# Kernel tuning notes

Hardware: AMD Instinct MI355X
Metric: run time of the kernel (lower is better)

Reference implementation:

```python
import jax, jax.numpy as jnp
import numpy as np

B, T, D, HS = 8, 2048, 1024, 64  # batch, seq, num_embd, head_size


def setup_inputs() -> dict:
    key = jax.random.key(0)
    kc, kq, kk, kv = jax.random.split(key, 4)
    return {
        "context": jax.random.normal(kc, (B, T, D), dtype=jnp.float32),
        "Wq": jax.random.normal(kq, (D, HS), dtype=jnp.float32) * (D ** -0.5),
        "Wk": jax.random.normal(kk, (D, HS), dtype=jnp.float32) * (D ** -0.5),
        "Wv": jax.random.normal(kv, (D, HS), dtype=jnp.float32) * (D ** -0.5),
    }


def reference(context, Wq, Wk, Wv):
    # context: [B, T, D]; projections: [B, T, HS]
    q = context @ Wq
    k = context @ Wk
    v = context @ Wv
    scale = k.shape[-1] ** -0.5
    # scores: [B, T, T], causal mask, stable softmax (dropout p=0 -> identity)
    wei = jnp.einsum("btd,bsd->bts", q, k) * scale
    t = wei.shape[-1]
    causal = jnp.tril(jnp.ones((t, t), dtype=bool))
    wei = jnp.where(causal, wei, -jnp.inf)
    wei = jax.nn.softmax(wei, axis=-1)
    return jnp.einsum("bts,bsh->bth", wei, v)
```

## Files before the change

### kernel.cpp

```cpp
#include <hip/hip_runtime.h>
#include <math.h>

#define BB 8
#define TT 2048
#define DD 1024
#define HSZ 64

typedef __bf16 bf16_t;
typedef bf16_t bf16x8 __attribute__((ext_vector_type(8)));
typedef bf16_t bf16x4 __attribute__((ext_vector_type(4)));
typedef float f32x4 __attribute__((ext_vector_type(4)));

#define MFMA16(A, B, C) __builtin_amdgcn_mfma_f32_16x16x32_bf16(A, B, C, 0, 0, 0)


__global__ __launch_bounds__(256) void wt_convert(
    const float* __restrict__ Wq, const float* __restrict__ Wk,
    const float* __restrict__ Wv, bf16_t* __restrict__ Wtf)
{
    int id = blockIdx.x * 256 + threadIdx.x;
    int j = id & 7;
    int lane = (id >> 3) & 63;
    int chunk = (id >> 9) & 31;
    int nt = id >> 14;
    int l16 = lane & 15, quad = lane >> 4;
    int k = chunk * 32 + quad * 8 + j;
    int col = nt * 16 + l16;
    int m = col >> 6, ncol = col & 63;
    const float* W = (m == 0) ? Wq : (m == 1) ? Wk : Wv;
    float scl = (m == 0) ? 0.18033688f : 1.0f;
    Wtf[id] = (bf16_t)(W[k * HSZ + ncol] * scl);
}

__global__ __launch_bounds__(256, 3) void qkv_proj(
    const float* __restrict__ ctx, const bf16_t* __restrict__ Wtf,
    bf16_t* __restrict__ Q, bf16_t* __restrict__ Kf, bf16_t* __restrict__ Vf)
{
    __shared__ f32x4 red[4][12][64];

    const int tid = threadIdx.x;
    const int w = tid >> 6, lane = tid & 63;
    const int quad = lane >> 4, l16 = lane & 15;
    const size_t row0 = (size_t)blockIdx.x * 16;
    const int k0 = w * 256;

    f32x4 acc[12];
    #pragma unroll
    for (int i = 0; i < 12; ++i) acc[i] = (f32x4){0.f, 0.f, 0.f, 0.f};

    const float* arow = ctx + (row0 + l16) * DD + k0 + quad * 8;

    float4 a0 = *(const float4*)(arow);
    float4 a1 = *(const float4*)(arow + 4);
    #pragma unroll
    for (int kc = 0; kc < 256; kc += 32) {
        bf16x8 af;
        af[0] = (bf16_t)a0.x; af[1] = (bf16_t)a0.y;
        af[2] = (bf16_t)a0.z; af[3] = (bf16_t)a0.w;
        af[4] = (bf16_t)a1.x; af[5] = (bf16_t)a1.y;
        af[6] = (bf16_t)a1.z; af[7] = (bf16_t)a1.w;
        if (kc + 32 < 256) {
            a0 = *(const float4*)(arow + kc + 32);
            a1 = *(const float4*)(arow + kc + 36);
        }
        const int chunk = (k0 + kc) >> 5;
        #pragma unroll
        for (int nt = 0; nt < 12; ++nt) {
            const bf16_t* wp = Wtf + (((size_t)nt * 32 + chunk) * 64 + lane) * 8;
            bf16x8 bfrag = *(const bf16x8*)wp;
            acc[nt] = MFMA16(af, bfrag, acc[nt]);
        }
    }

    #pragma unroll
    for (int nt = 0; nt < 12; ++nt) red[w][nt][lane] = acc[nt];
    __syncthreads();

    const int bb   = (int)(row0 >> 11);
    const int tloc = (int)(row0 & 2047);
    const int kt   = tloc >> 6;
    const int nn   = (tloc >> 4) & 3;

    #pragma unroll
    for (int i = 0; i < 3; ++i) {
        const int nt = w * 3 + i;
        f32x4 s = red[0][nt][lane];
        s += red[1][nt][lane];
        s += red[2][nt][lane];
        s += red[3][nt][lane];

        const int m = nt >> 2;
        if (m == 0) {
            const int col = (nt & 3) * 16 + l16;
            #pragma unroll
            for (int reg = 0; reg < 4; ++reg)
                Q[(row0 + quad * 4 + reg) * HSZ + col] = (bf16_t)s[reg];
        } else if (m == 1) {
            const int g = nt - 4;
            const int ks = g >> 1;
            const int quadf = (g & 1) * 2 + (l16 >> 3);
            const int jj = l16 & 7;
            const size_t fb = ((((size_t)bb * 32 + kt) * 4 + nn) * 2 + ks) * 512;
            #pragma unroll
            for (int reg = 0; reg < 4; ++reg)
                Kf[fb + (quadf * 16 + quad * 4 + reg) * 8 + jj] = (bf16_t)s[reg];
        } else {
            const int dt = nt - 8;
            const int t0 = tloc + quad * 4;
            const int ks = (t0 >> 5) & 1;
            const int quadf = (t0 >> 3) & 3;
            const int j0 = t0 & 7;
            const size_t fb = ((((size_t)bb * 32 + kt) * 2 + ks) * 4 + dt) * 512;
            bf16x4 v;
            #pragma unroll
            for (int reg = 0; reg < 4; ++reg) v[reg] = (bf16_t)s[reg];
            *(bf16x4*)(Vf + fb + (quadf * 16 + l16) * 8 + j0) = v;
        }
    }
}

__global__ __launch_bounds__(64, 3) void attn_kernel(
    const bf16_t* __restrict__ Q, const bf16_t* __restrict__ Kf,
    const bf16_t* __restrict__ Vf,
    float* __restrict__ Opart, float* __restrict__ Lpart)
{
    __shared__ bf16_t Ps[16][76];

    const int lane = threadIdx.x;
    const int quad = lane >> 4, l16 = lane & 15;

    const int z = blockIdx.x;
    const int b = z & 7, c = z >> 3;
    const int j = 127 - (c >> 2);
    const int seg = c & 3;
    const size_t base = (size_t)b * TT * HSZ;
    const int ntile = (j >> 2) + 1, jm = j & 3;

    const bf16_t* qp = Q + base + (size_t)(j * 16 + l16) * HSZ + quad * 8;
    bf16x8 qf0 = *(const bf16x8*)qp;
    bf16x8 qf1 = *(const bf16x8*)(qp + 32);

    bf16x8 onesf;
    {
        bf16_t e = (l16 == 0) ? (bf16_t)1.0f : (bf16_t)0.0f;
        #pragma unroll
        for (int i = 0; i < 8; ++i) onesf[i] = e;
    }

    f32x4 o[4];
    #pragma unroll
    for (int dt = 0; dt < 4; ++dt) o[dt] = (f32x4){0.f, 0.f, 0.f, 0.f};
    f32x4 lacc = (f32x4){0.f, 0.f, 0.f, 0.f};

    for (int kt = seg; kt < ntile; kt += 4) {
        const bool last = (kt == ntile - 1);
        const int nv = last ? jm + 1 : 4;
        const int ksm = (nv > 2) ? 2 : 1;

        const bf16_t* kbase = Kf + (((size_t)b * 32 + kt) * 8) * 512 + lane * 8;
        bf16x8 kf[8];
        #pragma unroll
        for (int n = 0; n < 4; ++n) {
            if (n < nv) {
                kf[2 * n]     = *(const bf16x8*)(kbase + (n * 2) * 512);
                kf[2 * n + 1] = *(const bf16x8*)(kbase + (n * 2 + 1) * 512);
            }
        }
        const bf16_t* vbase = Vf + (((size_t)b * 32 + kt) * 8) * 512 + lane * 8;
        bf16x8 vf[8];
        #pragma unroll
        for (int dt = 0; dt < 4; ++dt) {
            vf[2 * dt] = *(const bf16x8*)(vbase + dt * 512);
            if (ksm == 2) vf[2 * dt + 1] = *(const bf16x8*)(vbase + (4 + dt) * 512);
        }

        f32x4 sc[4];
        #pragma unroll
        for (int n = 0; n < 4; ++n) {
            if (n < nv) {
                f32x4 a = (f32x4){0.f, 0.f, 0.f, 0.f};
                a = MFMA16(qf0, kf[2 * n], a);
                a = MFMA16(qf1, kf[2 * n + 1], a);
                sc[n] = a;
            }
        }

        if (last) {
            #pragma unroll
            for (int n = 0; n < 4; ++n) {
                if (n < nv) {
                    #pragma unroll
                    for (int reg = 0; reg < 4; ++reg) {
                        bool masked = (n == jm) && (l16 > quad * 4 + reg);
                        float p = __builtin_amdgcn_exp2f(sc[n][reg]);
                        sc[n][reg] = masked ? 0.f : p;
                    }
                }
            }
        } else {
            #pragma unroll
            for (int n = 0; n < 4; ++n) {
                #pragma unroll
                for (int reg = 0; reg < 4; ++reg)
                    sc[n][reg] = __builtin_amdgcn_exp2f(sc[n][reg]);
            }
        }

        #pragma unroll
        for (int n = 0; n < 4; ++n) {
            #pragma unroll
            for (int reg = 0; reg < 4; ++reg) {
                float p = (n < nv) ? sc[n][reg] : 0.f;
                Ps[quad * 4 + reg][n * 16 + l16] = (bf16_t)p;
            }
        }
        bf16x8 pf0 = *(const bf16x8*)&Ps[l16][quad * 8];
        bf16x8 pf1 = *(const bf16x8*)&Ps[l16][32 + quad * 8];

        #pragma unroll
        for (int dt = 0; dt < 4; ++dt) {
            o[dt] = MFMA16(pf0, vf[2 * dt], o[dt]);
            if (ksm == 2) o[dt] = MFMA16(pf1, vf[2 * dt + 1], o[dt]);
        }
        lacc = MFMA16(pf0, onesf, lacc);
        if (ksm == 2) lacc = MFMA16(pf1, onesf, lacc);
    }

    float* op = Opart + (size_t)z * 16 * 64;
    #pragma unroll
    for (int dt = 0; dt < 4; ++dt) {
        #pragma unroll
        for (int reg = 0; reg < 4; ++reg)
            op[(quad * 4 + reg) * 64 + dt * 16 + l16] = o[dt][reg];
    }
    if (l16 == 0) {
        #pragma unroll
        for (int reg = 0; reg < 4; ++reg)
            Lpart[z * 16 + quad * 4 + reg] = lacc[reg];
    }
}

__global__ __launch_bounds__(256) void combine_kernel(
    const float* __restrict__ Opart, const float* __restrict__ Lpart,
    float* __restrict__ O)
{
    int gid = blockIdx.x * 256 + threadIdx.x;
    int col = gid & 63;
    int row = (gid >> 6) & 15;
    int j   = (gid >> 10) & 127;
    int b   = gid >> 17;
    int z0 = ((127 - j) * 4) * 8 + b;
    float l = 0.f, ov = 0.f;
    #pragma unroll
    for (int s = 0; s < 4; ++s) {
        l  += Lpart[(z0 + 8 * s) * 16 + row];
        ov += Opart[((size_t)(z0 + 8 * s) * 16 + row) * 64 + col];
    }
    O[((size_t)b * TT + j * 16 + row) * 64 + col] = ov / l;
}

extern "C" void kernel_launch(void* const* d_in, const int* in_sizes, int n_in,
                              void* d_out, int out_size, void* d_ws, size_t ws_size,
                              hipStream_t stream) {
    const float* ctx = (const float*)d_in[0];
    const float* Wq  = (const float*)d_in[1];
    const float* Wk  = (const float*)d_in[2];
    const float* Wv  = (const float*)d_in[3];
    float* out = (float*)d_out;

    const size_t NQ = (size_t)BB * TT * HSZ;
    bf16_t* Qw  = (bf16_t*)d_ws;
    bf16_t* Kfw = Qw + NQ;
    bf16_t* Vfw = Kfw + NQ;
    bf16_t* Wtf = Vfw + NQ;
    float*  Opart = (float*)(Wtf + 196608);
    float*  Lpart = Opart + (size_t)4096 * 1024;

    wt_convert<<<768, 256, 0, stream>>>(Wq, Wk, Wv, Wtf);
    qkv_proj<<<1024, 256, 0, stream>>>(ctx, Wtf, Qw, Kfw, Vfw);
    attn_kernel<<<4096, 64, 0, stream>>>(Qw, Kfw, Vfw, Opart, Lpart);
    combine_kernel<<<4096, 256, 0, stream>>>(Opart, Lpart, out);
}
```

Before: 141.6 us.

## Double-buffer weight fragments in QKV projection and K fragments in attention

The QKV projection now prefetches the next chunk's weight fragments into a second register buffer while the MFMAs for the current chunk run, and its occupancy hint drops from 3 to 2 to make room for the extra registers. The attention kernel splits its loop into two K-fragment buffers, loading the next tile's K fragments before processing the current one so global load latency overlaps with compute. The cost is higher register pressure and lower occupancy, which may reduce the latency hiding that came from having more waves resident.

```diff
diff --git a/kernel.cpp b/kernel.cpp
--- a/kernel.cpp
+++ b/kernel.cpp
@@ -32,7 +32,7 @@
     Wtf[id] = (bf16_t)(W[k * HSZ + ncol] * scl);
 }
 
-__global__ __launch_bounds__(256, 3) void qkv_proj(
+__global__ __launch_bounds__(256, 2) void qkv_proj(
     const float* __restrict__ ctx, const bf16_t* __restrict__ Wtf,
     bf16_t* __restrict__ Q, bf16_t* __restrict__ Kf, bf16_t* __restrict__ Vf)
 {
@@ -49,27 +49,40 @@
     for (int i = 0; i < 12; ++i) acc[i] = (f32x4){0.f, 0.f, 0.f, 0.f};
 
     const float* arow = ctx + (row0 + l16) * DD + k0 + quad * 8;
-
+    const bf16_t* wbase = Wtf + lane * 8;
+
+    bf16x8 bfr[2][12];
+    {
+        const int chunk0 = k0 >> 5;
+        #pragma unroll
+        for (int nt = 0; nt < 12; ++nt)
+            bfr[0][nt] = *(const bf16x8*)(wbase + ((size_t)nt * 32 + chunk0) * 512);
+    }
     float4 a0 = *(const float4*)(arow);
     float4 a1 = *(const float4*)(arow + 4);
+
     #pragma unroll
     for (int kc = 0; kc < 256; kc += 32) {
+        const int cur = (kc >> 5) & 1;
         bf16x8 af;
         af[0] = (bf16_t)a0.x; af[1] = (bf16_t)a0.y;
         af[2] = (bf16_t)a0.z; af[3] = (bf16_t)a0.w;
         af[4] = (bf16_t)a1.x; af[5] = (bf16_t)a1.y;
         af[6] = (bf16_t)a1.z; af[7] = (bf16_t)a1.w;
+
         if (kc + 32 < 256) {
+            const int chunk = (k0 + kc + 32) >> 5;
+            #pragma unroll
+            for (int nt = 0; nt < 12; ++nt)
+                bfr[cur ^ 1][nt] =
+                    *(const bf16x8*)(wbase + ((size_t)nt * 32 + chunk) * 512);
             a0 = *(const float4*)(arow + kc + 32);
             a1 = *(const float4*)(arow + kc + 36);
         }
-        const int chunk = (k0 + kc) >> 5;
-        #pragma unroll
-        for (int nt = 0; nt < 12; ++nt) {
-            const bf16_t* wp = Wtf + (((size_t)nt * 32 + chunk) * 64 + lane) * 8;
-            bf16x8 bfrag = *(const bf16x8*)wp;
-            acc[nt] = MFMA16(af, bfrag, acc[nt]);
-        }
+
+        #pragma unroll
+        for (int nt = 0; nt < 12; ++nt)
+            acc[nt] = MFMA16(af, bfr[cur][nt], acc[nt]);
     }
 
     #pragma unroll
@@ -119,6 +132,20 @@
     }
 }
 
+__device__ __forceinline__ void load_kfrags(
+    const bf16_t* __restrict__ Kf, size_t bofs, int kt, int lane, int nv,
+    bf16x8* kf)
+{
+    const bf16_t* kbase = Kf + ((bofs + (size_t)kt) * 8) * 512 + lane * 8;
+    #pragma unroll
+    for (int n = 0; n < 4; ++n) {
+        if (n < nv) {
+            kf[2 * n]     = *(const bf16x8*)(kbase + (n * 2) * 512);
+            kf[2 * n + 1] = *(const bf16x8*)(kbase + (n * 2 + 1) * 512);
+        }
+    }
+}
+
 __global__ __launch_bounds__(64, 3) void attn_kernel(
     const bf16_t* __restrict__ Q, const bf16_t* __restrict__ Kf,
     const bf16_t* __restrict__ Vf,
@@ -134,6 +161,7 @@
     const int j = 127 - (c >> 2);
     const int seg = c & 3;
     const size_t base = (size_t)b * TT * HSZ;
+    const size_t bofs = (size_t)b * 32;
     const int ntile = (j >> 2) + 1, jm = j & 3;
 
     const bf16_t* qp = Q + base + (size_t)(j * 16 + l16) * HSZ + quad * 8;
@@ -152,21 +180,14 @@
     for (int dt = 0; dt < 4; ++dt) o[dt] = (f32x4){0.f, 0.f, 0.f, 0.f};
     f32x4 lacc = (f32x4){0.f, 0.f, 0.f, 0.f};
 
-    for (int kt = seg; kt < ntile; kt += 4) {
+    bf16x8 kA[8], kB[8];
+
+    auto process = [&](int kt, const bf16x8* kf) {
         const bool last = (kt == ntile - 1);
         const int nv = last ? jm + 1 : 4;
         const int ksm = (nv > 2) ? 2 : 1;
 
-        const bf16_t* kbase = Kf + (((size_t)b * 32 + kt) * 8) * 512 + lane * 8;
-        bf16x8 kf[8];
-        #pragma unroll
-        for (int n = 0; n < 4; ++n) {
-            if (n < nv) {
-                kf[2 * n]     = *(const bf16x8*)(kbase + (n * 2) * 512);
-                kf[2 * n + 1] = *(const bf16x8*)(kbase + (n * 2 + 1) * 512);
-            }
-        }
-        const bf16_t* vbase = Vf + (((size_t)b * 32 + kt) * 8) * 512 + lane * 8;
+        const bf16_t* vbase = Vf + ((bofs + (size_t)kt) * 8) * 512 + lane * 8;
         bf16x8 vf[8];
         #pragma unroll
         for (int dt = 0; dt < 4; ++dt) {
@@ -199,11 +220,10 @@
             }
         } else {
             #pragma unroll
-            for (int n = 0; n < 4; ++n) {
+            for (int n = 0; n < 4; ++n)
                 #pragma unroll
                 for (int reg = 0; reg < 4; ++reg)
                     sc[n][reg] = __builtin_amdgcn_exp2f(sc[n][reg]);
-            }
         }
 
         #pragma unroll
@@ -224,6 +244,20 @@
         }
         lacc = MFMA16(pf0, onesf, lacc);
         if (ksm == 2) lacc = MFMA16(pf1, onesf, lacc);
+    };
+
+    auto nv_of = [&](int kt) { return (kt == ntile - 1) ? jm + 1 : 4; };
+
+    if (seg < ntile) {
+        load_kfrags(Kf, bofs, seg, lane, nv_of(seg), kA);
+        for (int kt = seg; kt < ntile; kt += 8) {
+            if (kt + 4 < ntile) load_kfrags(Kf, bofs, kt + 4, lane, nv_of(kt + 4), kB);
+            process(kt, kA);
+            if (kt + 4 < ntile) {
+                if (kt + 8 < ntile) load_kfrags(Kf, bofs, kt + 8, lane, nv_of(kt + 8), kA);
+                process(kt + 4, kB);
+            }
+        }
     }
 
     float* op = Opart + (size_t)z * 16 * 64;
```

Result: no change. 140.4 us (-0.9%).
